# Optimization experiments

Hardware: AMD Instinct MI355X
Metric: run time of the kernel (lower is better)

## Reference

```python
import jax, jax.numpy as jnp
import numpy as np

B, S, NGB, NG, DIM = 64, 4096, 13, 48, 3
NCH = [8, 8, 1]
NSHELLS = 8


def setup_inputs() -> dict:
    key = jax.random.key(0)
    ks = jax.random.split(key, 16)
    rng = np.random.default_rng(0)
    # valid row-wise permutations of the N_ngb neighbor slots per group op
    GnnPerms = jnp.asarray(np.argsort(rng.random((NG, NGB)), axis=1), dtype=jnp.int64)
    NNSites = jax.random.randint(ks[0], (NGB, S), 0, S, dtype=jnp.int64)
    SitesToShells = jax.random.randint(ks[1], (S,), 0, NSHELLS, dtype=jnp.int64)
    # block-diagonal (Ng*dim, Ng*dim) cartesian rotation blocks
    blk = rng.normal(size=(NG, DIM, DIM)).astype(np.float32) * 0.5
    gd = np.zeros((NG * DIM, NG * DIM), np.float32)
    for g in range(NG):
        gd[g * DIM:(g + 1) * DIM, g * DIM:(g + 1) * DIM] = blk[g]
    gdiags = jnp.asarray(gd)
    std = 0.2
    return {
        "InStates": jax.random.normal(ks[2], (B, 1, S), jnp.float32),
        "Psi0": jax.random.normal(ks[3], (NCH[0], 1, NGB), jnp.float32) * std,
        "bias0": jax.random.normal(ks[4], (NCH[0], 1), jnp.float32) * std,
        "Psi1": jax.random.normal(ks[5], (NCH[1], NCH[0], NGB), jnp.float32) * std,
        "bias1": jax.random.normal(ks[6], (NCH[1], 1), jnp.float32) * std,
        "Psi2": jax.random.normal(ks[7], (NCH[2], NCH[1], NGB), jnp.float32) * std,
        "bias2": jax.random.normal(ks[8], (NCH[2], 1), jnp.float32) * std,
        "wtVC": jax.random.normal(ks[9], (DIM, NGB), jnp.float32) * std,
        "ShellWeights": jax.random.normal(ks[10], (NSHELLS,), jnp.float32) * std,
        "gdiags": gdiags,
        "GnnPerms": GnnPerms,
        "NNSites": NNSites,
        "SitesToShells": SitesToShells,
    }


def _rearrange(x, NNSites):
    # x: (B, Nch, S) -> (B, Nch*N_ngb, S); subchannel j of channel c holds x[b, c, NNSites[j, s]]
    b, c, s = x.shape
    return x[:, :, NNSites].reshape(b, c * NGB, s)


def _gconv(x, W, b):
    # x: (B, NchIn*N_ngb, S); W: (NchOut, NchIn, N_ngb); b: (NchOut, 1)
    # group-rotated weights: GW[o, g, c*N_ngb+j] = W[o, c, GnnPerms[g, j]]
    GW = _gconv.GW_cache  # set per-call below via closure-free pattern; replaced in reference
    raise NotImplementedError


def reference(InStates, Psi0, bias0, Psi1, bias1, Psi2, bias2, wtVC,
              ShellWeights, gdiags, GnnPerms, NNSites, SitesToShells):
    act = jax.nn.softplus

    def gconv(x, W, b):
        # rotated weights: (NchOut, Ng, NchIn*N_ngb)
        GW = W[:, :, GnnPerms].transpose(0, 2, 1, 3).reshape(W.shape[0], NG, -1)
        h = jnp.einsum('ogk,bks->bogs', GW, x) + b[:, :, None]  # (B, NchOut, Ng, S)
        return act(h).mean(axis=2)                               # group-orbit average

    out = _rearrange(InStates, NNSites)
    for W, b in ((Psi0, bias0), (Psi1, bias1), (Psi2, bias2)):
        out = gconv(out, W, b)                 # (B, NchOut, S)
        out = _rearrange(out, NNSites)         # (B, NchOut*N_ngb, S)
    # vector channel: row g*dim+d of P is wtVC[d, GnnPerms[g]]
    P = wtVC[:, GnnPerms].transpose(1, 0, 2).reshape(NG * DIM, NGB)
    Wvc = gdiags @ P                           # (Ng*dim, N_ngb)
    v = jnp.einsum('kn,bns->bks', Wvc, out)    # (B, Ng*dim, S)
    v = v.reshape(-1, NG, DIM, out.shape[-1]).mean(axis=1)  # (B, dim, S)
    v = v * ShellWeights[SitesToShells]        # per-site shell weighting
    return v.sum(axis=2) / out.shape[-1]       # (B, dim)
```

## Files before the change

kernel.cpp:

```cpp
#include <hip/hip_runtime.h>
#include <hip/hip_bf16.h>

#define BATCH 64
#define SITES 4096
#define NGB 13
#define NGRP 48
#define SDIM 3

typedef __bf16 bf16x8 __attribute__((ext_vector_type(8)));
typedef __bf16 bf16x4 __attribute__((ext_vector_type(4)));
typedef float  f32x4  __attribute__((ext_vector_type(4)));

#define OFF_AVC  0
#define OFF_U    64
#define OFF_A0   67648
#define OFF_A1   2164800
#define OFF_PART 4261952
#define UW0H 0
#define UW0L 12288
#define UW1H 24576
#define UW1L 73728
#define UW2H 122880
#define UW2L 129024

__device__ __forceinline__ float softplus_f(float h) {
    return fmaxf(h, 0.f) + __logf(1.f + __expf(-fabsf(h)));
}

__global__ __launch_bounds__(256) void precompute_kernel(
    const float* __restrict__ Psi0, const float* __restrict__ Psi1,
    const float* __restrict__ Psi2, const float* __restrict__ wtVC,
    const float* __restrict__ gdiags, const int* __restrict__ perms,
    float* __restrict__ ws)
{
    float*  Avc = ws + OFF_AVC;
    __bf16* U   = (__bf16*)(ws + OFF_U);
    int t = blockIdx.x * 256 + threadIdx.x;
    if (t < 12288) {
        int k = t & 31, row = t >> 5;
        int o = row / NGRP, g = row - o * NGRP;
        float w = (k < NGB) ? Psi0[o * NGB + perms[g * NGB + k]] : 0.f;
        __bf16 hi = (__bf16)w;
        U[UW0H + t] = hi;
        U[UW0L + t] = (__bf16)(w - (float)hi);
    } else if (t < 61440) {
        int u = t - 12288;
        int k = u & 127, row = u >> 7;
        int o = row / NGRP, g = row - o * NGRP;
        float w = 0.f;
        if (k < 104) { int c = k / NGB, j = k - c * NGB;
                       w = Psi1[(o * 8 + c) * NGB + perms[g * NGB + j]]; }
        __bf16 hi = (__bf16)w;
        U[UW1H + u] = hi;
        U[UW1L + u] = (__bf16)(w - (float)hi);
    } else if (t < 67584) {
        int u = t - 61440;
        int k = u & 127, g = u >> 7;
        float w = 0.f;
        if (k < 104) { int c = k / NGB, j = k - c * NGB;
                       w = Psi2[c * NGB + perms[g * NGB + j]]; }
        __bf16 hi = (__bf16)w;
        U[UW2H + u] = hi;
        U[UW2L + u] = (__bf16)(w - (float)hi);
    } else if (t < 67584 + 39 * NGRP) {
        int t2 = t - 67584;
        int g = t2 % NGRP, u = t2 / NGRP;
        int d = u / NGB, n = u % NGB;
        const int row = g * SDIM + d;
        float s = 0.f;
        for (int k = 0; k < NGRP * SDIM; k++) {
            int g2 = k / SDIM, d2 = k - g2 * SDIM;
            float p = wtVC[d2 * NGB + perms[g2 * NGB + n]];
            s = fmaf(gdiags[row * (NGRP * SDIM) + k], p, s);
        }
        atomicAdd(&Avc[u], s * (1.f / 48.f));
    }
}

template<int NCIN, int NCTOT, int CT, int KPAD, int NWN>
__global__ __launch_bounds__(512) void layer_mfma(
    const float* __restrict__ prev,
    const __bf16* __restrict__ Wh,
    const __bf16* __restrict__ Wl,
    const float* __restrict__ bias,
    const int*   __restrict__ NN,
    float* __restrict__ out)
{
    constexpr int K      = NCIN * NGB;
    constexpr int M      = NCTOT * NGRP;
    constexpr int MTILES = M / 16, NTILES = CT / 16;
    constexpr int NWM    = 8 / NWN;
    constexpr int MT_W   = MTILES / NWM, NT_W = NTILES / NWN;
    constexpr int KT     = KPAD / 32;
    constexpr int KSTR   = KPAD + 4;

    static_assert(MT_W * 16 == NGRP, "wave covers exactly one o");
    static_assert(NWM * MT_W == MTILES && NWN * NT_W == NTILES, "");
    static_assert((KPAD & 31) == 0, "");

    __shared__ __bf16 xh_lds[CT * KSTR];
    __shared__ __bf16 xl_lds[CT * KSTR];

    const int tid  = threadIdx.x;
    const int wave = tid >> 6, lane = tid & 63;
    const int m16  = lane & 15, quad = lane >> 4;

    const int b  = blockIdx.x / (SITES / CT);
    const int s0 = (blockIdx.x % (SITES / CT)) * CT;

    for (int site = tid; site < NGB * CT; site += 512) {
        int j = site / CT, col = site % CT;
        int nn = NN[j * SITES + s0 + col];
        if constexpr (NCIN == 1) {
            float v = prev[(size_t)b * SITES + nn];
            __bf16 hi = (__bf16)v;
            xh_lds[col * KSTR + j] = hi;
            xl_lds[col * KSTR + j] = (__bf16)(v - (float)hi);
        } else {
            const float4* p4 = (const float4*)(prev + ((size_t)(b * SITES + nn)) * 8);
            float4 u0 = p4[0], u1 = p4[1];
            float v[8] = {u0.x, u0.y, u0.z, u0.w, u1.x, u1.y, u1.z, u1.w};
#pragma unroll
            for (int c = 0; c < 8; c++) {
                int k = c * NGB + j;
                __bf16 hi = (__bf16)v[c];
                xh_lds[col * KSTR + k] = hi;
                xl_lds[col * KSTR + k] = (__bf16)(v[c] - (float)hi);
            }
        }
    }
    for (int e = tid; e < CT * (KPAD - K); e += 512) {
        int col = e / (KPAD - K), p = e - col * (KPAD - K);
        xh_lds[col * KSTR + K + p] = (__bf16)0.f;
        xl_lds[col * KSTR + K + p] = (__bf16)0.f;
    }
    __syncthreads();

    const int wave_mt0 = (wave / NWN) * MT_W;
    const int wave_nt0 = (wave % NWN) * NT_W;
    const int o_g      = (wave_mt0 * 16) / NGRP;

    f32x4 acc[MT_W][NT_W];
#pragma unroll
    for (int mt = 0; mt < MT_W; mt++)
#pragma unroll
        for (int nt = 0; nt < NT_W; nt++) acc[mt][nt] = (f32x4){0.f, 0.f, 0.f, 0.f};

#pragma unroll 1
    for (int kt = 0; kt < KT; kt++) {
        const int koff = kt * 32 + quad * 8;
        bf16x8 ah[MT_W], al[MT_W];
#pragma unroll
        for (int mt = 0; mt < MT_W; mt++) {
            int row = (wave_mt0 + mt) * 16 + m16;
            ah[mt] = *(const bf16x8*)(Wh + (size_t)row * KPAD + koff);
            al[mt] = *(const bf16x8*)(Wl + (size_t)row * KPAD + koff);
        }
#pragma unroll
        for (int nt = 0; nt < NT_W; nt++) {
            int cbase = ((wave_nt0 + nt) * 16 + m16) * KSTR + koff;
            bf16x4 h0 = *(const bf16x4*)(xh_lds + cbase);
            bf16x4 h1 = *(const bf16x4*)(xh_lds + cbase + 4);
            bf16x4 l0 = *(const bf16x4*)(xl_lds + cbase);
            bf16x4 l1 = *(const bf16x4*)(xl_lds + cbase + 4);
            bf16x8 bh = __builtin_shufflevector(h0, h1, 0, 1, 2, 3, 4, 5, 6, 7);
            bf16x8 bl = __builtin_shufflevector(l0, l1, 0, 1, 2, 3, 4, 5, 6, 7);
#pragma unroll
            for (int mt = 0; mt < MT_W; mt++) {
                acc[mt][nt] = __builtin_amdgcn_mfma_f32_16x16x32_bf16(
                    ah[mt], bh, acc[mt][nt], 0, 0, 0);
                acc[mt][nt] = __builtin_amdgcn_mfma_f32_16x16x32_bf16(
                    al[mt], bh, acc[mt][nt], 0, 0, 0);
                acc[mt][nt] = __builtin_amdgcn_mfma_f32_16x16x32_bf16(
                    ah[mt], bl, acc[mt][nt], 0, 0, 0);
            }
        }
    }

    const float bo = bias[o_g];
#pragma unroll
    for (int nt = 0; nt < NT_W; nt++) {
        float s = 0.f;
#pragma unroll
        for (int mt = 0; mt < MT_W; mt++)
#pragma unroll
            for (int r = 0; r < 4; r++)
                s += softplus_f(acc[mt][nt][r] + bo);
        s += __shfl_xor(s, 16);
        s += __shfl_xor(s, 32);
        if (quad == 0)
            out[((size_t)(b * SITES + s0 + (wave_nt0 + nt) * 16 + m16)) * NCTOT + o_g]
                = s * (1.f / 48.f);
    }
}

__global__ __launch_bounds__(256) void reduce_a(
    const float* __restrict__ A2, const int* __restrict__ NN,
    const int* __restrict__ s2sh, const float* __restrict__ sw,
    const float* __restrict__ Avc, float* __restrict__ partial)
{
    const int b = blockIdx.x >> 4;
    const int chunk = blockIdx.x & 15;
    const int tid = threadIdx.x;
    const int s = (chunk << 8) + tid;
    const float* a = A2 + (size_t)b * SITES;

    float y0 = 0.f, y1 = 0.f, y2 = 0.f;
#pragma unroll
    for (int n = 0; n < NGB; n++) {
        float v = a[NN[n * SITES + s]];
        y0 = fmaf(Avc[n],           v, y0);
        y1 = fmaf(Avc[NGB + n],     v, y1);
        y2 = fmaf(Avc[2 * NGB + n], v, y2);
    }
    const float wgt = sw[s2sh[s]];
    y0 *= wgt; y1 *= wgt; y2 *= wgt;

    __shared__ float red[3][256];
    red[0][tid] = y0; red[1][tid] = y1; red[2][tid] = y2;
    __syncthreads();
    for (int st = 128; st > 0; st >>= 1) {
        if (tid < st) {
            red[0][tid] += red[0][tid + st];
            red[1][tid] += red[1][tid + st];
            red[2][tid] += red[2][tid + st];
        }
        __syncthreads();
    }
    if (tid < 3) partial[(b * 16 + chunk) * 3 + tid] = red[tid][0];
}

__global__ __launch_bounds__(256) void reduce_b(
    const float* __restrict__ partial, float* __restrict__ out)
{
    int t = threadIdx.x;
    if (t < BATCH * 3) {
        int b = t / 3, d = t - b * 3;
        float s = 0.f;
        for (int c = 0; c < 16; c++) s += partial[(b * 16 + c) * 3 + d];
        out[t] = s * (1.f / (float)SITES);
    }
}

extern "C" void kernel_launch(void* const* d_in, const int* in_sizes, int n_in,
                              void* d_out, int out_size, void* d_ws, size_t ws_size,
                              hipStream_t stream)
{
    const float* InStates = (const float*)d_in[0];
    const float* Psi0     = (const float*)d_in[1];
    const float* bias0    = (const float*)d_in[2];
    const float* Psi1     = (const float*)d_in[3];
    const float* bias1    = (const float*)d_in[4];
    const float* Psi2     = (const float*)d_in[5];
    const float* bias2    = (const float*)d_in[6];
    const float* wtVC     = (const float*)d_in[7];
    const float* ShellW   = (const float*)d_in[8];
    const float* gdiags   = (const float*)d_in[9];
    const int*   GnnPerms = (const int*)d_in[10];
    const int*   NNSites  = (const int*)d_in[11];
    const int*   S2Sh     = (const int*)d_in[12];

    float*  ws   = (float*)d_ws;
    float*  Avc  = ws + OFF_AVC;
    __bf16* U    = (__bf16*)(ws + OFF_U);
    float*  A0   = ws + OFF_A0;
    float*  A1   = ws + OFF_A1;
    float*  A2   = ws + OFF_A0;
    float*  PART = ws + OFF_PART;

    float* out = (float*)d_out;

    hipMemsetAsync(Avc, 0, 39 * sizeof(float), stream);
    precompute_kernel<<<272, 256, 0, stream>>>(Psi0, Psi1, Psi2, wtVC, gdiags,
                                               GnnPerms, ws);

    layer_mfma<1, 8, 64, 32, 1><<<BATCH * (SITES / 64), 512, 0, stream>>>(
        InStates, U + UW0H, U + UW0L, bias0, NNSites, A0);
    layer_mfma<8, 8, 64, 128, 1><<<BATCH * (SITES / 64), 512, 0, stream>>>(
        A0, U + UW1H, U + UW1L, bias1, NNSites, A1);
    layer_mfma<8, 1, 128, 128, 8><<<BATCH * (SITES / 128), 512, 0, stream>>>(
        A1, U + UW2H, U + UW2L, bias2, NNSites, A2);

    reduce_a<<<BATCH * 16, 256, 0, stream>>>(A2, NNSites, S2Sh, ShellW, Avc, PART);
    reduce_b<<<1, 256, 0, stream>>>(PART, out);
}
```

Baseline: 387.0 us.

## Interleave K as neighbor-major channel-minor for vectorized LDS staging and loads

Reorders the K dimension of layers 1 and 2 from channel-major (c*13+j) to neighbor-major (j*8+c), in both the precomputed weights and the LDS tile. Each gathered neighbor's 8 channels can then be written as one 16-byte bf16x8 store instead of 8 scattered scalar stores. The LDS stride is padded to a multiple of 8 so B fragments load as single 16-byte reads, and the K loop is fully unrolled with all B fragments loaded before the MFMA block. Layer 2 changes from 128-site, 512-thread blocks to 64-site, 256-thread blocks, which may change bank-conflict behaviour and register pressure.

```diff
diff --git a/kernel.cpp b/kernel.cpp
--- a/kernel.cpp
+++ b/kernel.cpp
@@ -8,7 +8,6 @@
 #define SDIM 3
 
 typedef __bf16 bf16x8 __attribute__((ext_vector_type(8)));
-typedef __bf16 bf16x4 __attribute__((ext_vector_type(4)));
 typedef float  f32x4  __attribute__((ext_vector_type(4)));
 
 #define OFF_AVC  0
@@ -48,7 +47,7 @@
         int k = u & 127, row = u >> 7;
         int o = row / NGRP, g = row - o * NGRP;
         float w = 0.f;
-        if (k < 104) { int c = k / NGB, j = k - c * NGB;
+        if (k < 104) { int j = k >> 3, c = k & 7;
                        w = Psi1[(o * 8 + c) * NGB + perms[g * NGB + j]]; }
         __bf16 hi = (__bf16)w;
         U[UW1H + u] = hi;
@@ -57,7 +56,7 @@
         int u = t - 61440;
         int k = u & 127, g = u >> 7;
         float w = 0.f;
-        if (k < 104) { int c = k / NGB, j = k - c * NGB;
+        if (k < 104) { int j = k >> 3, c = k & 7;
                        w = Psi2[c * NGB + perms[g * NGB + j]]; }
         __bf16 hi = (__bf16)w;
         U[UW2H + u] = hi;
@@ -77,8 +76,8 @@
     }
 }
 
-template<int NCIN, int NCTOT, int CT, int KPAD, int NWN>
-__global__ __launch_bounds__(512) void layer_mfma(
+template<int NCIN, int NCTOT, int CT, int KPAD, int KSTR, int NWAVES, int NWN>
+__global__ __launch_bounds__(NWAVES * 64) void layer_mfma(
     const float* __restrict__ prev,
     const __bf16* __restrict__ Wh,
     const __bf16* __restrict__ Wl,
@@ -86,17 +85,17 @@
     const int*   __restrict__ NN,
     float* __restrict__ out)
 {
+    constexpr int NTHR   = NWAVES * 64;
     constexpr int K      = NCIN * NGB;
     constexpr int M      = NCTOT * NGRP;
     constexpr int MTILES = M / 16, NTILES = CT / 16;
-    constexpr int NWM    = 8 / NWN;
+    constexpr int NWM    = NWAVES / NWN;
     constexpr int MT_W   = MTILES / NWM, NT_W = NTILES / NWN;
     constexpr int KT     = KPAD / 32;
-    constexpr int KSTR   = KPAD + 4;
 
     static_assert(MT_W * 16 == NGRP, "wave covers exactly one o");
     static_assert(NWM * MT_W == MTILES && NWN * NT_W == NTILES, "");
-    static_assert((KPAD & 31) == 0, "");
+    static_assert((KPAD & 31) == 0 && (KSTR & 7) == 0, "");
 
     __shared__ __bf16 xh_lds[CT * KSTR];
     __shared__ __bf16 xl_lds[CT * KSTR];
@@ -108,31 +107,43 @@
     const int b  = blockIdx.x / (SITES / CT);
     const int s0 = (blockIdx.x % (SITES / CT)) * CT;
 
-    for (int site = tid; site < NGB * CT; site += 512) {
-        int j = site / CT, col = site % CT;
-        int nn = NN[j * SITES + s0 + col];
-        if constexpr (NCIN == 1) {
+    if constexpr (NCIN == 1) {
+        for (int site = tid; site < NGB * CT; site += NTHR) {
+            int j = site / CT, col = site % CT;
+            int nn = NN[j * SITES + s0 + col];
             float v = prev[(size_t)b * SITES + nn];
             __bf16 hi = (__bf16)v;
             xh_lds[col * KSTR + j] = hi;
             xl_lds[col * KSTR + j] = (__bf16)(v - (float)hi);
-        } else {
+        }
+        for (int e = tid; e < CT * (KPAD - NGB); e += NTHR) {
+            int col = e / (KPAD - NGB), p = e % (KPAD - NGB);
+            xh_lds[col * KSTR + NGB + p] = (__bf16)0.f;
+            xl_lds[col * KSTR + NGB + p] = (__bf16)0.f;
+        }
+    } else {
+        for (int site = tid; site < NGB * CT; site += NTHR) {
+            int j = site / CT, col = site % CT;
+            int nn = NN[j * SITES + s0 + col];
             const float4* p4 = (const float4*)(prev + ((size_t)(b * SITES + nn)) * 8);
             float4 u0 = p4[0], u1 = p4[1];
             float v[8] = {u0.x, u0.y, u0.z, u0.w, u1.x, u1.y, u1.z, u1.w};
+            bf16x8 hv, lv;
 #pragma unroll
             for (int c = 0; c < 8; c++) {
-                int k = c * NGB + j;
                 __bf16 hi = (__bf16)v[c];
-                xh_lds[col * KSTR + k] = hi;
-                xl_lds[col * KSTR + k] = (__bf16)(v[c] - (float)hi);
+                hv[c] = hi;
+                lv[c] = (__bf16)(v[c] - (float)hi);
             }
-        }
-    }
-    for (int e = tid; e < CT * (KPAD - K); e += 512) {
-        int col = e / (KPAD - K), p = e - col * (KPAD - K);
-        xh_lds[col * KSTR + K + p] = (__bf16)0.f;
-        xl_lds[col * KSTR + K + p] = (__bf16)0.f;
+            *(bf16x8*)(xh_lds + col * KSTR + j * 8) = hv;
+            *(bf16x8*)(xl_lds + col * KSTR + j * 8) = lv;
+        }
+        const bf16x8 z8 = {};
+        for (int e = tid; e < CT * 3; e += NTHR) {
+            int col = e % CT, z = e / CT;
+            *(bf16x8*)(xh_lds + col * KSTR + 104 + z * 8) = z8;
+            *(bf16x8*)(xl_lds + col * KSTR + 104 + z * 8) = z8;
+        }
     }
     __syncthreads();
 
@@ -146,10 +157,10 @@
 #pragma unroll
         for (int nt = 0; nt < NT_W; nt++) acc[mt][nt] = (f32x4){0.f, 0.f, 0.f, 0.f};
 
-#pragma unroll 1
+#pragma unroll
     for (int kt = 0; kt < KT; kt++) {
         const int koff = kt * 32 + quad * 8;
-        bf16x8 ah[MT_W], al[MT_W];
+        bf16x8 ah[MT_W], al[MT_W], bh[NT_W], bl[NT_W];
 #pragma unroll
         for (int mt = 0; mt < MT_W; mt++) {
             int row = (wave_mt0 + mt) * 16 + m16;
@@ -159,22 +170,20 @@
 #pragma unroll
         for (int nt = 0; nt < NT_W; nt++) {
             int cbase = ((wave_nt0 + nt) * 16 + m16) * KSTR + koff;
-            bf16x4 h0 = *(const bf16x4*)(xh_lds + cbase);
-            bf16x4 h1 = *(const bf16x4*)(xh_lds + cbase + 4);
-            bf16x4 l0 = *(const bf16x4*)(xl_lds + cbase);
-            bf16x4 l1 = *(const bf16x4*)(xl_lds + cbase + 4);
-            bf16x8 bh = __builtin_shufflevector(h0, h1, 0, 1, 2, 3, 4, 5, 6, 7);
-            bf16x8 bl = __builtin_shufflevector(l0, l1, 0, 1, 2, 3, 4, 5, 6, 7);
-#pragma unroll
-            for (int mt = 0; mt < MT_W; mt++) {
+            bh[nt] = *(const bf16x8*)(xh_lds + cbase);
+            bl[nt] = *(const bf16x8*)(xl_lds + cbase);
+        }
+#pragma unroll
+        for (int mt = 0; mt < MT_W; mt++)
+#pragma unroll
+            for (int nt = 0; nt < NT_W; nt++) {
                 acc[mt][nt] = __builtin_amdgcn_mfma_f32_16x16x32_bf16(
-                    ah[mt], bh, acc[mt][nt], 0, 0, 0);
+                    ah[mt], bh[nt], acc[mt][nt], 0, 0, 0);
                 acc[mt][nt] = __builtin_amdgcn_mfma_f32_16x16x32_bf16(
-                    al[mt], bh, acc[mt][nt], 0, 0, 0);
+                    al[mt], bh[nt], acc[mt][nt], 0, 0, 0);
                 acc[mt][nt] = __builtin_amdgcn_mfma_f32_16x16x32_bf16(
-                    ah[mt], bl, acc[mt][nt], 0, 0, 0);
+                    ah[mt], bl[nt], acc[mt][nt], 0, 0, 0);
             }
-        }
     }
 
     const float bo = bias[o_g];
@@ -274,11 +283,11 @@
     precompute_kernel<<<272, 256, 0, stream>>>(Psi0, Psi1, Psi2, wtVC, gdiags,
                                                GnnPerms, ws);
 
-    layer_mfma<1, 8, 64, 32, 1><<<BATCH * (SITES / 64), 512, 0, stream>>>(
+    layer_mfma<1, 8, 64, 32, 40, 8, 1><<<BATCH * (SITES / 64), 512, 0, stream>>>(
         InStates, U + UW0H, U + UW0L, bias0, NNSites, A0);
-    layer_mfma<8, 8, 64, 128, 1><<<BATCH * (SITES / 64), 512, 0, stream>>>(
+    layer_mfma<8, 8, 64, 128, 136, 8, 1><<<BATCH * (SITES / 64), 512, 0, stream>>>(
         A0, U + UW1H, U + UW1L, bias1, NNSites, A1);
-    layer_mfma<8, 1, 128, 128, 8><<<BATCH * (SITES / 128), 512, 0, stream>>>(
+    layer_mfma<8, 1, 64, 128, 136, 4, 4><<<BATCH * (SITES / 64), 256, 0, stream>>>(
         A1, U + UW2H, U + UW2L, bias2, NNSites, A2);
 
     reduce_a<<<BATCH * 16, 256, 0, stream>>>(A2, NNSites, S2Sh, ShellW, Avc, PART);
```

Result: faster. 376.7 us (-2.7%).
